# Performance work log

Hardware: AMD Instinct MI355X
Metric: run time of the kernel (lower is better)

## Reference

```python
import jax, jax.numpy as jnp
import numpy as np

THETA = 10.0      # spike threshold
TAU_SR = 1.0      # SRM (psp) kernel time constant
TAU_REF = 1.0     # refractory kernel time constant
SCALE_REF = 2.0   # refractory kernel scale (SLAYER default: -2*theta peak)


@jax.custom_vjp
def spike_fn(v):
    # Heaviside on (membrane - theta); surrogate gradient in bwd (SLAYER-style pdf)
    return (v >= 0.0).astype(v.dtype)

def _spike_fwd(v):
    return spike_fn(v), v

def _spike_bwd(v, g):
    return (g * jnp.exp(-jnp.abs(v) / THETA) / THETA,)

spike_fn.defvjp(_spike_fwd, _spike_bwd)


def alpha_psp(x, tau):
    """Causal conv of x (T, B, F) with alpha kernel eps[k] = (k/tau)*exp(1-k/tau),
    implemented as a 2-state linear recurrence (exact for the discrete kernel)."""
    d = jnp.float32(np.exp(-1.0 / tau))
    c = jnp.float32(np.e / tau)

    def step(carry, xt):
        p, q = carry
        q = d * (q + p)          # q[t] = sum_s x[s]*(t-s)*d^(t-s)
        p = d * p + xt           # p[t] = sum_s x[s]*d^(t-s)
        return (p, q), c * q

    z = jnp.zeros_like(x[0])
    _, out = jax.lax.scan(step, (z, z), x)
    return out


def spike_dyn(u, tau_ref, scale_ref, theta):
    """Threshold-with-refractory dynamics. u: (T, B, F) synaptic drive.
    membrane[t] = u[t] - scale_ref*theta * (alpha refractory conv of past spikes)."""
    d = jnp.float32(np.exp(-1.0 / tau_ref))
    c = jnp.float32(np.e / tau_ref)
    cref = jnp.float32(-scale_ref * theta) * c

    def step(carry, ut):
        p, q = carry
        q = d * (q + p)                       # refractory trace (lag-0 coeff is 0)
        s = spike_fn(ut + cref * q - theta)   # spike if membrane >= theta
        p = d * p + s
        return (p, q), s

    z = jnp.zeros_like(u[0])
    _, s = jax.lax.scan(step, (z, z), u)
    return s


def setup_inputs() -> dict:
    key = jax.random.key(0)
    k1, k2, k3 = jax.random.split(key, 3)
    # sparse binary input spike trains, (B, C, H, W, T) SLAYER layout
    downsampled = (jax.random.uniform(k1, (16, 2, 50, 63, 500)) < 0.1).astype(jnp.float32)
    w1 = jax.random.normal(k2, (1024, 6300), dtype=jnp.float32) * 0.1
    w2 = jax.random.normal(k3, (20, 1024), dtype=jnp.float32) * 0.1
    return {"downsampled": downsampled, "w1": w1, "w2": w2}


def reference(downsampled, w1, w2):
    B, T = downsampled.shape[0], downsampled.shape[-1]
    x = downsampled.reshape(B, -1, T).transpose(2, 0, 1)   # (T, B, 6300)
    p1 = alpha_psp(x, TAU_SR)                              # psp filter
    u1 = jnp.einsum('tbf,of->tbo', p1, w1)                 # fc1 (per-timestep dense)
    s1 = spike_dyn(u1, TAU_REF, SCALE_REF, THETA)          # spike layer 1
    p2 = alpha_psp(s1, TAU_SR)
    u2 = jnp.einsum('tbh,oh->tbo', p2, w2)                 # fc2
    s2 = spike_dyn(u2, TAU_REF, SCALE_REF, THETA)
    return s2.transpose(1, 2, 0)                           # (B, output_size, T)
```

## Files before the change

### kernel.cpp

```cpp
#include <hip/hip_runtime.h>
#include <cstdint>
#include <cstddef>

#define T_N   500
#define B_N   16
#define F_IN  6300
#define KW    198
#define KPAD  6336
#define H1    1024
#define H2    20
#define N2P   32
#define M_N   8000
#define M_PADN 8064

#define DD_C   0.36787944117144233f
#define CC_C   2.718281828459045f
#define THETA_C 10.0f
#define INV2048 4.8828125e-4f

typedef _Float16 half8 __attribute__((ext_vector_type(8)));
typedef __attribute__((ext_vector_type(4))) float f32x4;

__device__ __forceinline__ unsigned short f2h_bits(float x) {
    union { _Float16 h; unsigned short u; } c; c.h = (_Float16)x; return c.u;
}
__device__ __forceinline__ float h2f(unsigned short u) {
    union { _Float16 h; unsigned short u; } c; c.u = u; return (float)c.h;
}

__global__ void prep_fused_k(const float* __restrict__ x,
                             const float* __restrict__ w1,
                             const float* __restrict__ w2,
                             uint32_t* __restrict__ bits_t,
                             unsigned short* __restrict__ w1f,
                             unsigned short* __restrict__ w2f) {
    const int bid = blockIdx.x;
    if (bid < 6336) {
        const int b    = bid & 15;
        const int tmp  = bid >> 4;
        const int w    = tmp % 198;
        const int tch2 = tmp / 198;
        const int t    = tch2 * 256 + threadIdx.x;
        if (t >= 504) return;
        const int m = t * 16 + b;
        uint32_t word = 0u;
        if (t < T_N) {
            const int fbase = w * 32;
            #pragma unroll
            for (int j = 0; j < 32; ++j) {
                const int f = fbase + j;
                float v = 0.f;
                if (f < F_IN) v = x[((size_t)b * F_IN + f) * T_N + t];
                word |= (v != 0.f ? 1u : 0u) << j;
            }
        }
        bits_t[(size_t)w * M_PADN + m] = word;
    } else if (bid < 6336 + 1024) {
        const int o = bid - 6336;
        #pragma unroll 1
        for (int it = 0; it < 25; ++it) {
            const int f = it * 256 + threadIdx.x;
            if (f >= KPAD) break;
            float w = (f < F_IN) ? w1[(size_t)o * F_IN + f] : 0.f;
            const unsigned short h1 = f2h_bits(w);
            const float r1 = w - h2f(h1);
            const unsigned short h2 = f2h_bits(r1 * 2048.0f);
            const size_t base = (size_t)o * KPAD + f;
            w1f[base]                     = h1;
            w1f[(size_t)H1 * KPAD + base] = h2;
        }
    } else {
        const int o = bid - 7360;
        #pragma unroll
        for (int it = 0; it < 4; ++it) {
            const int k = it * 256 + threadIdx.x;
            float w = (o < H2) ? w2[(size_t)o * H1 + k] : 0.f;
            const unsigned short h1 = f2h_bits(w);
            const float r1 = w - h2f(h1);
            const unsigned short h2 = f2h_bits(r1 * 2048.0f);
            const size_t base = (size_t)o * H1 + k;
            w2f[base]                    = h1;
            w2f[(size_t)N2P * H1 + base] = h2;
        }
    }
}

__global__ __launch_bounds__(256, 2)
void gemm1_mfma_k(const uint32_t* __restrict__ bits_t,
                  const unsigned short* __restrict__ w1f,
                  float* __restrict__ u1) {
    __shared__ uint32_t BsU[2][2 * 128 * 16];

    const int tid  = threadIdx.x;
    const int lane = tid & 63;
    const int wave = tid >> 6;
    const int n0 = blockIdx.x * 128;
    const int m0 = blockIdx.y * 128;
    const int l15 = lane & 15, g = lane >> 4;

    const unsigned short* bsrc0 =
        w1f + (size_t)(n0 + (lane >> 2)) * KPAD + ((lane & 3) ^ ((lane >> 3) & 3)) * 8;

    const uint32_t* pbits = bits_t + m0 + l15;

    f32x4 acc[2][8][2];
    const f32x4 fz = {0.f, 0.f, 0.f, 0.f};
    #pragma unroll
    for (int t = 0; t < 2; ++t)
        #pragma unroll
        for (int mi = 0; mi < 8; ++mi)
            #pragma unroll
            for (int ni = 0; ni < 2; ++ni) acc[t][mi][ni] = fz;

    int boff[2];
    #pragma unroll
    for (int ni = 0; ni < 2; ++ni) {
        const int br = wave * 32 + ni * 16 + l15;
        boff[ni] = br * 16 + ((g ^ ((br >> 1) & 3)) << 2);
    }

#define STAGE_B(tt, bb)                                                        \
    {                                                                          \
        _Pragma("unroll")                                                      \
        for (int j = 0; j < 4; ++j) {                                          \
            const int e    = wave * 4 + j;                          \
            const int term = e >> 3;                                           \
            const int ii   = e & 7;                           \
            const unsigned short* src =                                        \
                bsrc0 + (size_t)(term * H1 + ii * 16) * KPAD + (size_t)(tt) * 32; \
            __builtin_amdgcn_global_load_lds(                                  \
                (const __attribute__((address_space(1))) uint32_t*)src,        \
                (__attribute__((address_space(3))) uint32_t*)&BsU[bb][term * 2048 + ii * 256], \
                16, 0, 0);                                                     \
        }                                                                      \
    }

#define LOAD_W(W, tt)                                                          \
    {                                                                          \
        const uint32_t* p = pbits + (size_t)(tt) * M_PADN;                     \
        _Pragma("unroll")                                                      \
        for (int mi = 0; mi < 8; ++mi) W[mi] = p[mi * 16];                     \
    }

#define COMPUTE(W, bb)                                                         \
    {                                                                          \
        half8 bf0[2], bf1[2];                                                  \
        _Pragma("unroll")                                                      \
        for (int ni = 0; ni < 2; ++ni) {                                       \
            bf0[ni] = *(const half8*)&BsU[bb][boff[ni]];                       \
            bf1[ni] = *(const half8*)&BsU[bb][2048 + boff[ni]];                \
        }                                                                      \
        __builtin_amdgcn_s_setprio(1);                                         \
        _Pragma("unroll")                                                      \
        for (int mi = 0; mi < 8; ++mi) {                                       \
            const uint32_t w8 = W[mi] >> (g * 8);                              \
            union { uint32_t u[4]; half8 h; } cv;                              \
            _Pragma("unroll")                                                  \
            for (int i = 0; i < 4; ++i)                                        \
                cv.u[i] = ((((w8 >> (2 * i)) & 3u) * 0x8001u) & 0x10001u)      \
                          * 0x3C00u;                                           \
            _Pragma("unroll")                                                  \
            for (int ni = 0; ni < 2; ++ni) {                                   \
                acc[0][mi][ni] = __builtin_amdgcn_mfma_f32_16x16x32_f16(       \
                    cv.h, bf0[ni], acc[0][mi][ni], 0, 0, 0);                   \
                acc[1][mi][ni] = __builtin_amdgcn_mfma_f32_16x16x32_f16(       \
                    cv.h, bf1[ni], acc[1][mi][ni], 0, 0, 0);                   \
            }                                                                  \
        }                                                                      \
        __builtin_amdgcn_s_setprio(0);                                         \
    }

#define ITER(tt, cb, WCUR, WNEXT)                                              \
    {                                                                          \
        LOAD_W(WNEXT, (tt) + 1);                                               \
        STAGE_B((tt) + 1, (cb) ^ 1);                                           \
        COMPUTE(WCUR, cb);                                                     \
        __syncthreads();                                                       \
    }

    uint32_t wA[8], wB[8];
    LOAD_W(wA, 0);
    STAGE_B(0, 0);
    __syncthreads();

    for (int t = 0; t < KW - 2; t += 2) {
        ITER(t,     0, wA, wB);
        ITER(t + 1, 1, wB, wA);
    }
    ITER(KW - 2, 0, wA, wB);
    COMPUTE(wB, 1);

#undef ITER
#undef COMPUTE
#undef LOAD_W
#undef STAGE_B

    #pragma unroll
    for (int mi = 0; mi < 8; ++mi) {
        const int mbase = m0 + mi * 16 + g * 4;
        #pragma unroll
        for (int ni = 0; ni < 2; ++ni) {
            const int o = n0 + wave * 32 + ni * 16 + l15;
            #pragma unroll
            for (int r = 0; r < 4; ++r)
                u1[(size_t)(mbase + r) * H1 + o] =
                    acc[0][mi][ni][r] + acc[1][mi][ni][r] * INV2048;
        }
    }
}

__global__ void scan1_k(const float* __restrict__ u1, unsigned short* __restrict__ s1f) {
    const int lane = blockIdx.x * 64 + threadIdx.x;
    const float CREF = -20.0f * CC_C;
    float p1 = 0.f, q1 = 0.f, pr = 0.f, qr = 0.f;
    float A[10], Bv[10];

#define STEP1(xv, tidx) {                                   \
        q1 = DD_C * (q1 + p1); p1 = DD_C * p1 + (xv);       \
        const float uu = CC_C * q1;                         \
        qr = DD_C * (qr + pr);                              \
        const float vv = uu + CREF * qr - THETA_C;          \
        const float ss = (vv >= 0.f) ? 1.f : 0.f;           \
        pr = DD_C * pr + ss;                                \
        s1f[(size_t)(tidx) * 16384 + lane] =                \
            (vv >= 0.f) ? (unsigned short)0x3C00 : (unsigned short)0; }

    #pragma unroll
    for (int j = 0; j < 10; ++j) A[j] = u1[(size_t)j * 16384 + lane];
    for (int it = 0; it < 25; ++it) {
        const int gB = 2 * it + 1;
        #pragma unroll
        for (int j = 0; j < 10; ++j) Bv[j] = u1[(size_t)(gB * 10 + j) * 16384 + lane];
        #pragma unroll
        for (int j = 0; j < 10; ++j) STEP1(A[j], (2 * it) * 10 + j);
        if (it < 24) {
            const int gA = 2 * it + 2;
            #pragma unroll
            for (int j = 0; j < 10; ++j) A[j] = u1[(size_t)(gA * 10 + j) * 16384 + lane];
        }
        #pragma unroll
        for (int j = 0; j < 10; ++j) STEP1(Bv[j], gB * 10 + j);
    }
#undef STEP1
}

__global__ __launch_bounds__(256)
void gemm2_mfma_k(const unsigned short* __restrict__ s1f,
                  const unsigned short* __restrict__ w2f,
                  float* __restrict__ u2p) {
    __shared__ uint32_t AsU[128 * 16];
    __shared__ uint32_t BsU[2 * 32 * 16];

    const int tid  = threadIdx.x;
    const int lane = tid & 63;
    const int wave = tid >> 6;
    const int m0 = blockIdx.x * 128;
    const int kc = blockIdx.y;
    const int l15 = lane & 15, g = lane >> 4;

    f32x4 acc[2][2][2];
    const f32x4 fz = {0.f, 0.f, 0.f, 0.f};
    #pragma unroll
    for (int t = 0; t < 2; ++t)
        #pragma unroll
        for (int i = 0; i < 2; ++i)
            #pragma unroll
            for (int j = 0; j < 2; ++j) acc[t][i][j] = fz;

    int aoff[2], boff[2][2];
    #pragma unroll
    for (int mi = 0; mi < 2; ++mi) {
        const int ar = wave * 32 + mi * 16 + l15;
        aoff[mi] = ar * 16 + ((g ^ ((ar >> 1) & 3)) << 2);
    }
    #pragma unroll
    for (int term = 0; term < 2; ++term)
        #pragma unroll
        for (int ni = 0; ni < 2; ++ni) {
            const int br = ni * 16 + l15;
            boff[term][ni] = term * 512 + br * 16 + ((g ^ ((br >> 1) & 3)) << 2);
        }

    for (int kw8 = 0; kw8 < 8; ++kw8) {
        const int kw = kc * 8 + kw8;
        __syncthreads();
        #pragma unroll
        for (int i = 0; i < 2; ++i) {
            const int c   = i * 256 + tid;
            const int row = c >> 2;
            const int kch = c & 3;
            const unsigned short* src =
                s1f + (size_t)(m0 + row) * H1 + kw * 32 + (kch ^ ((row >> 1) & 3)) * 8;
            __builtin_amdgcn_global_load_lds(
                (const __attribute__((address_space(1))) uint32_t*)src,
                (__attribute__((address_space(3))) uint32_t*)&AsU[(i * 256 + wave * 64) * 4],
                16, 0, 0);
        }
        {
            const int c    = tid;
            const int term = c >> 7;
            const int o    = (c >> 2) & 31;
            const int kch  = c & 3;
            const unsigned short* src =
                w2f + (size_t)(term * N2P + o) * H1 + kw * 32 + (kch ^ ((o >> 1) & 3)) * 8;
            __builtin_amdgcn_global_load_lds(
                (const __attribute__((address_space(1))) uint32_t*)src,
                (__attribute__((address_space(3))) uint32_t*)&BsU[wave * 256],
                16, 0, 0);
        }
        __syncthreads();

        half8 af[2];
        #pragma unroll
        for (int mi = 0; mi < 2; ++mi) af[mi] = *(const half8*)&AsU[aoff[mi]];
        #pragma unroll
        for (int term = 0; term < 2; ++term)
            #pragma unroll
            for (int ni = 0; ni < 2; ++ni) {
                const half8 bf = *(const half8*)&BsU[boff[term][ni]];
                #pragma unroll
                for (int mi = 0; mi < 2; ++mi)
                    acc[term][mi][ni] = __builtin_amdgcn_mfma_f32_16x16x32_f16(
                        af[mi], bf, acc[term][mi][ni], 0, 0, 0);
            }
    }

    #pragma unroll
    for (int mi = 0; mi < 2; ++mi) {
        const int mbase = m0 + wave * 32 + mi * 16 + g * 4;
        #pragma unroll
        for (int ni = 0; ni < 2; ++ni) {
            const int o = ni * 16 + l15;
            #pragma unroll
            for (int r = 0; r < 4; ++r)
                u2p[((size_t)kc * M_PADN + mbase + r) * N2P + o] =
                    acc[0][mi][ni][r] + acc[1][mi][ni][r] * INV2048;
        }
    }
}

__global__ void sum_u2_k(const float* __restrict__ u2p, float* __restrict__ u2) {
    const int i = blockIdx.x * 256 + threadIdx.x;
    const size_t P = (size_t)M_PADN * N2P;
    u2[i] = (u2p[i] + u2p[P + i]) + (u2p[2 * P + i] + u2p[3 * P + i]);
}

__global__ void scan2_k(const float* __restrict__ u2, float* __restrict__ out) {
    const int lane = blockIdx.x * 64 + threadIdx.x;
    if (lane >= 320) return;
    const int b  = lane / 20;
    const int o2 = lane % 20;
    const int boffs = b * N2P + o2;
    const float CREF = -20.0f * CC_C;
    float p1 = 0.f, q1 = 0.f, pr = 0.f, qr = 0.f;
    float A[10], Bv[10];

#define LOAD2(tidx) (u2[(size_t)(tidx) * 512 + boffs])

#define STEP2(xv, tidx) {                                   \
        q1 = DD_C * (q1 + p1); p1 = DD_C * p1 + (xv);       \
        const float uu = CC_C * q1;                         \
        qr = DD_C * (qr + pr);                              \
        const float vv = uu + CREF * qr - THETA_C;          \
        const float ss = (vv >= 0.f) ? 1.f : 0.f;           \
        pr = DD_C * pr + ss;                                \
        out[(size_t)lane * T_N + (tidx)] = ss; }

    #pragma unroll
    for (int j = 0; j < 10; ++j) A[j] = LOAD2(j);
    for (int it = 0; it < 25; ++it) {
        const int gB = 2 * it + 1;
        #pragma unroll
        for (int j = 0; j < 10; ++j) Bv[j] = LOAD2(gB * 10 + j);
        #pragma unroll
        for (int j = 0; j < 10; ++j) STEP2(A[j], (2 * it) * 10 + j);
        if (it < 24) {
            const int gA = 2 * it + 2;
            #pragma unroll
            for (int j = 0; j < 10; ++j) A[j] = LOAD2(gA * 10 + j);
        }
        #pragma unroll
        for (int j = 0; j < 10; ++j) STEP2(Bv[j], gB * 10 + j);
    }
#undef STEP2
#undef LOAD2
}

extern "C" void kernel_launch(void* const* d_in, const int* in_sizes, int n_in,
                              void* d_out, int out_size, void* d_ws, size_t ws_size,
                              hipStream_t stream) {
    const float* x  = (const float*)d_in[0];
    const float* w1 = (const float*)d_in[1];
    const float* w2 = (const float*)d_in[2];
    float* out = (float*)d_out;

    char* ws = (char*)d_ws;
    size_t off = 0;
    uint32_t*       bits_t = (uint32_t*)(ws + off);       off += (size_t)KW * M_PADN * 4;
    unsigned short* w1f    = (unsigned short*)(ws + off); off += (size_t)2 * H1 * KPAD * 2;
    unsigned short* w2f    = (unsigned short*)(ws + off); off += (size_t)2 * N2P * H1 * 2;
    float*          u1     = (float*)(ws + off);          off += (size_t)M_PADN * H1 * 4;
    unsigned short* s1f    = (unsigned short*)(ws + off); off += (size_t)M_PADN * H1 * 2;
    float*          u2p    = (float*)(ws + off);          off += (size_t)4 * M_PADN * N2P * 4;
    float*          u2     = (float*)(ws + off);          off += (size_t)M_PADN * N2P * 4;
    (void)ws_size; (void)in_sizes; (void)n_in; (void)out_size;

    prep_fused_k <<<7392,        256, 0, stream>>>(x, w1, w2, bits_t, w1f, w2f);
    gemm1_mfma_k <<<dim3(8, 63), 256, 0, stream>>>(bits_t, w1f, u1);
    scan1_k      <<<256,         64,  0, stream>>>(u1, s1f);
    gemm2_mfma_k <<<dim3(63, 4), 256, 0, stream>>>(s1f, w2f, u2p);
    sum_u2_k     <<<1008,        256, 0, stream>>>(u2p, u2);
    scan2_k      <<<5,           64,  0, stream>>>(u2, out);
}
```

Before: 331.6 us.

## Triple-buffer GEMM1 B tiles with prefetch distance two and partial vmcnt waits

Moves the fc1 MFMA GEMM's shared-memory staging of weight tiles from double to triple buffering. Tiles are prefetched two iterations ahead, and __syncthreads is replaced by an explicit s_waitcnt vmcnt(N) plus s_barrier, so loads for later tiles stay in flight across the barrier. This aims to hide global-load latency behind MFMA compute. In exchange it uses 50% more LDS, which may reduce occupancy at 2 blocks per CU, and correctness depends on the hand-counted vmcnt values.

```diff
diff --git a/kernel.cpp b/kernel.cpp
--- a/kernel.cpp
+++ b/kernel.cpp
@@ -89,7 +89,7 @@
 void gemm1_mfma_k(const uint32_t* __restrict__ bits_t,
                   const unsigned short* __restrict__ w1f,
                   float* __restrict__ u1) {
-    __shared__ uint32_t BsU[2][2 * 128 * 16];
+    __shared__ uint32_t BsU[3][2 * 128 * 16];
 
     const int tid  = threadIdx.x;
     const int lane = tid & 63;
@@ -170,27 +170,47 @@
         __builtin_amdgcn_s_setprio(0);                                         \
     }
 
-#define ITER(tt, cb, WCUR, WNEXT)                                              \
+#define CBAR(NN)                                                               \
+    __builtin_amdgcn_sched_barrier(0);                                         \
+    asm volatile("s_waitcnt vmcnt(" #NN ")" ::: "memory");                     \
+    __builtin_amdgcn_s_barrier();                                              \
+    __builtin_amdgcn_sched_barrier(0);
+
+#define ONE(tt, bb, WCUR, WNEXT)                                               \
     {                                                                          \
+        STAGE_B((tt) + 2, ((bb) + 2) % 3);                                     \
         LOAD_W(WNEXT, (tt) + 1);                                               \
-        STAGE_B((tt) + 1, (cb) ^ 1);                                           \
-        COMPUTE(WCUR, cb);                                                     \
-        __syncthreads();                                                       \
+        COMPUTE(WCUR, bb);                                                     \
+        CBAR(12)                                                               \
     }
 
     uint32_t wA[8], wB[8];
+    STAGE_B(0, 0);
+    STAGE_B(1, 1);
     LOAD_W(wA, 0);
-    STAGE_B(0, 0);
-    __syncthreads();
-
-    for (int t = 0; t < KW - 2; t += 2) {
-        ITER(t,     0, wA, wB);
-        ITER(t + 1, 1, wB, wA);
-    }
-    ITER(KW - 2, 0, wA, wB);
-    COMPUTE(wB, 1);
-
-#undef ITER
+    CBAR(12)
+
+    for (int t = 0; t < 192; t += 6) {
+        ONE(t,     0, wA, wB);
+        ONE(t + 1, 1, wB, wA);
+        ONE(t + 2, 2, wA, wB);
+        ONE(t + 3, 0, wB, wA);
+        ONE(t + 4, 1, wA, wB);
+        ONE(t + 5, 2, wB, wA);
+    }
+    ONE(192, 0, wA, wB);
+    ONE(193, 1, wB, wA);
+    ONE(194, 2, wA, wB);
+    ONE(195, 0, wB, wA);
+    {
+        LOAD_W(wB, 197);
+        COMPUTE(wA, 1);
+        CBAR(8)
+    }
+    COMPUTE(wB, 2);
+
+#undef ONE
+#undef CBAR
 #undef COMPUTE
 #undef LOAD_W
 #undef STAGE_B
```

After: 363.7 us. 1.1x slower.
